# Performance work log

Measured on AMD Instinct MI355X. Metric: run time of the kernel, lower is better.

The kernel has to match this reference:

```python
import jax, jax.numpy as jnp
import numpy as np

B, QL, T, H = 32, 1, 2048, 512


def setup_inputs() -> dict:
    key = jax.random.key(0)
    ks = jax.random.split(key, 10)
    n = lambda i, shape, sc=1.0: jax.random.normal(ks[i], shape, dtype=jnp.float32) * sc
    inv = 1.0 / np.sqrt(H)
    return {
        "query": n(0, (B, QL, H)),
        "value": n(1, (B, T, H)),
        "last_attn": jax.random.uniform(ks[2], (B, T), dtype=jnp.float32),
        "conv_w": n(3, (H, 1, 3), 0.1),   # Conv1d weight (out_ch, in_ch=1, k=3)
        "conv_b": n(4, (H,), 0.1),
        "q_w": n(5, (H, H), inv),          # query_proj (no bias)
        "v_w": n(6, (H, H), inv),          # value_proj (no bias)
        "s_w": n(7, (1, H), inv),          # score_proj weight
        "s_b": n(8, (1,), 0.1),            # score_proj bias
        "bias": n(9, (H,), 0.1),           # learned additive bias
    }


def reference(query, value, last_attn, conv_w, conv_b, q_w, v_w, s_w, s_b, bias):
    Tlen = last_attn.shape[1]
    # Conv1d(in=1, out=H, k=3, pad=1) over last_attn, then transpose -> (B, T, H)
    pad = jnp.pad(last_attn, ((0, 0), (1, 1)))
    frames = jnp.stack([pad[:, k:k + Tlen] for k in range(3)], axis=0)  # (3, B, T)
    conv_attn = jnp.einsum('hk,kbt->bth', conv_w[:, 0, :], frames) + conv_b  # (B, T, H)
    q = jnp.einsum('bqh,oh->bqo', query, q_w)   # (B, 1, H)
    v = jnp.einsum('bth,oh->bto', value, v_w)   # (B, T, H)
    e = jnp.tanh(q + v + conv_attn + bias)      # (B, T, H), q broadcasts over T
    score = jnp.einsum('bth,oh->bt', e, s_w) + s_b  # (B, T)
    # smoothing=True branch: sigmoid then L1-normalize
    score = jax.nn.sigmoid(score)
    attn = score / jnp.sum(score, axis=-1, keepdims=True)
    context = jnp.einsum('bt,bth->bh', attn, value)  # bmm(attn[:,None,:], value).squeeze(1)
    return context, attn
```

## Files before the change

### kernel.cpp

```cpp
#include <hip/hip_runtime.h>
#include <math.h>

#define B 32
#define T 2048
#define H 512

#define BT2 64
#define ASTR 520

typedef __attribute__((ext_vector_type(8))) __bf16 bf16x8;
typedef __attribute__((ext_vector_type(4))) __bf16 bf16x4v;
typedef __attribute__((ext_vector_type(4))) float f32x4;
typedef __attribute__((ext_vector_type(4))) float floatx4;

union pack8 { bf16x4v h; uint2 u; };

__global__ __launch_bounds__(256) void k_init(const float* __restrict__ query,
                                              const float* __restrict__ q_w,
                                              const float* __restrict__ bias,
                                              const float* __restrict__ v_w,
                                              float* __restrict__ qpb,
                                              unsigned short* __restrict__ wbf,
                                              float* __restrict__ ctx_num,
                                              float* __restrict__ denom) {
    const int blk = blockIdx.x;
    const int tid = threadIdx.x;

    if (blk >= 544) {
#pragma unroll
        for (int i = 0; i < 16; ++i) {
            const int off = tid * 4 + i * 1024;
            *(f32x4*)(ctx_num + off) = (f32x4){0.f, 0.f, 0.f, 0.f};
        }
        if (tid < B) denom[tid] = 0.f;
        return;
    }
    if (blk >= 512) {
        const int c2 = blk - 512;
        const int wv = tid >> 6;
        const int lane = tid & 63;
        const int srow = (c2 >> 2) * 64 + (c2 & 3) * 16 + (lane & 15);
        const int scol0 = (lane >> 4) * 8;
#pragma unroll
        for (int kk = 0; kk < 4; ++kk) {
            const int k = wv * 4 + kk;
            const float* src = v_w + (size_t)srow * H + k * 32 + scol0;
            f32x4 a0 = __builtin_nontemporal_load((const f32x4*)src);
            f32x4 a1 = __builtin_nontemporal_load((const f32x4*)(src + 4));
            pack8 p0, p1;
            p0.h = __builtin_convertvector(a0, bf16x4v);
            p1.h = __builtin_convertvector(a1, bf16x4v);
            uint4 u = {p0.u.x, p0.u.y, p1.u.x, p1.u.y};
            *(uint4*)(wbf + ((size_t)c2 * 16 + k) * 512 + lane * 8) = u;
        }
        return;
    }

    const int b = blk >> 4;
    const int s = blk & 15;
    const int wave = tid >> 6;
    const int lane = tid & 63;

    const float* qb = query + (size_t)b * H + lane * 8;
    f32x4 q0 = *(const f32x4*)qb;
    f32x4 q1 = *(const f32x4*)(qb + 4);

    const int o0 = s * 32 + wave * 8;
#pragma unroll
    for (int i = 0; i < 8; ++i) {
        const int o = o0 + i;
        const float* wr = q_w + (size_t)o * H + lane * 8;
        f32x4 w0 = __builtin_nontemporal_load((const f32x4*)wr);
        f32x4 w1 = __builtin_nontemporal_load((const f32x4*)(wr + 4));
        float acc = w0.x * q0.x + w0.y * q0.y + w0.z * q0.z + w0.w * q0.w +
                    w1.x * q1.x + w1.y * q1.y + w1.z * q1.z + w1.w * q1.w;
#pragma unroll
        for (int m = 1; m < 64; m <<= 1) acc += __shfl_xor(acc, m);
        if (lane == 0) qpb[b * H + o] = acc + bias[o];
    }
}

__global__ __launch_bounds__(512, 4) void k2_fused(const float* __restrict__ value,
                                                   const unsigned short* __restrict__ wbf,
                                                   const float* __restrict__ la,
                                                   const float* __restrict__ conv_w,
                                                   const float* __restrict__ conv_b,
                                                   const float* __restrict__ s_w,
                                                   const float* __restrict__ qpb,
                                                   const float* __restrict__ s_b,
                                                   float* __restrict__ pre_sg,
                                                   float* __restrict__ ctx_num,
                                                   float* __restrict__ denom) {
    __shared__ __align__(16) unsigned short As[BT2 * ASTR];
    __shared__ float las[BT2 + 2];
    __shared__ float redp[BT2][9];
    __shared__ float sgs[BT2];
    __shared__ float redc[4][H];

    const int t0 = blockIdx.x * BT2;
    const int b  = blockIdx.y;
    const int tid = threadIdx.x;
    const int wave = tid >> 6;
    const int lane = tid & 63;
    const int tx   = lane & 15;
    const int quad = lane >> 4;
    const int wn   = wave * 64;

    if (tid < BT2 + 2) {
        const int t = t0 + tid - 1;
        las[tid] = (t >= 0 && t < T) ? la[b * T + t] : 0.f;
    }

    {
        const int srow = tid >> 3;
        const int scol = (tid & 7) * 8;
        const float* sg = value + ((size_t)b * T + t0 + srow) * H + scol;
        unsigned short* sl = &As[srow * ASTR + scol];
#pragma unroll
        for (int c = 0; c < 8; ++c) {
            f32x4 a0 = __builtin_nontemporal_load((const f32x4*)(sg + c * 64));
            f32x4 a1 = __builtin_nontemporal_load((const f32x4*)(sg + c * 64 + 4));
            pack8 p0, p1;
            p0.h = __builtin_convertvector(a0, bf16x4v);
            p1.h = __builtin_convertvector(a1, bf16x4v);
            uint4 u = {p0.u.x, p0.u.y, p1.u.x, p1.u.y};
            *(uint4*)(sl + c * 64) = u;
        }
    }
    __syncthreads();

    floatx4 acc[4][4];
#pragma unroll
    for (int i = 0; i < 4; ++i)
#pragma unroll
        for (int j = 0; j < 4; ++j) acc[i][j] = (floatx4){0.f, 0.f, 0.f, 0.f};

    const unsigned short* gB = wbf + (size_t)wave * 32768 + lane * 8;
    const unsigned short* aB = &As[tx * ASTR + quad * 8];

    bf16x8 bcur[4], bnxt[4];
#pragma unroll
    for (int ni = 0; ni < 4; ++ni)
        bcur[ni] = *(const bf16x8*)(gB + ni * 8192);

#pragma unroll
    for (int k = 0; k < 16; ++k) {
        if (k < 15) {
#pragma unroll
            for (int ni = 0; ni < 4; ++ni)
                bnxt[ni] = *(const bf16x8*)(gB + ni * 8192 + (k + 1) * 512);
        }
        bf16x8 af[4];
#pragma unroll
        for (int mi = 0; mi < 4; ++mi)
            af[mi] = *(const bf16x8*)(aB + mi * 16 * ASTR + k * 32);
#pragma unroll
        for (int mi = 0; mi < 4; ++mi)
#pragma unroll
            for (int ni = 0; ni < 4; ++ni)
                acc[mi][ni] = __builtin_amdgcn_mfma_f32_16x16x32_bf16(
                    af[mi], bcur[ni], acc[mi][ni], 0, 0, 0);
        if (k < 15) {
#pragma unroll
            for (int ni = 0; ni < 4; ++ni) bcur[ni] = bnxt[ni];
        }
    }

    float qp4[4], sw4[4], cb4[4], c04[4], c14[4], c24[4];
#pragma unroll
    for (int ni = 0; ni < 4; ++ni) {
        const int ol = wn + ni * 16 + tx;
        qp4[ni] = qpb[b * H + ol];
        sw4[ni] = s_w[ol];
        cb4[ni] = conv_b[ol];
        c04[ni] = conv_w[ol * 3 + 0];
        c14[ni] = conv_w[ol * 3 + 1];
        c24[ni] = conv_w[ol * 3 + 2];
    }

    float sacc[16];
#pragma unroll
    for (int i = 0; i < 16; ++i) sacc[i] = 0.f;
#pragma unroll
    for (int ni = 0; ni < 4; ++ni) {
#pragma unroll
        for (int mi = 0; mi < 4; ++mi)
#pragma unroll
            for (int r = 0; r < 4; ++r) {
                const int tl = mi * 16 + quad * 4 + r;
                const float conv = c04[ni] * las[tl] + c14[ni] * las[tl + 1] +
                                   c24[ni] * las[tl + 2] + cb4[ni];
                const float x = acc[mi][ni][r] + qp4[ni] + conv;
                const float ex = __expf(2.f * x);
                const float th = 1.f - 2.f * __builtin_amdgcn_rcpf(ex + 1.f);
                sacc[mi * 4 + r] += sw4[ni] * th;
            }
    }
#pragma unroll
    for (int i = 0; i < 16; ++i) {
        float v = sacc[i];
        v += __shfl_xor(v, 1);
        v += __shfl_xor(v, 2);
        v += __shfl_xor(v, 4);
        v += __shfl_xor(v, 8);
        if (tx == 0) redp[(i >> 2) * 16 + quad * 4 + (i & 3)][wave] = v;
    }
    __syncthreads();

    if (tid < BT2) {
        float sc = s_b[0];
#pragma unroll
        for (int w = 0; w < 8; ++w) sc += redp[tid][w];
        const float sg = 1.f / (1.f + __expf(-sc));
        sgs[tid] = sg;
        pre_sg[b * T + t0 + tid] = sg;
        float dsum = sg;
#pragma unroll
        for (int m = 1; m < 64; m <<= 1) dsum += __shfl_xor(dsum, m);
        if (tid == 0) atomicAdd(&denom[b], dsum);
    }
    __syncthreads();

    {
        const int h4 = (tid & 127) * 4;
        const int tp = tid >> 7;
        f32x4 a = {0.f, 0.f, 0.f, 0.f};
        for (int t = tp; t < BT2; t += 4) {
            const float w = sgs[t];
            bf16x4v hv = *(const bf16x4v*)&As[t * ASTR + h4];
            f32x4 v = __builtin_convertvector(hv, f32x4);
            a.x += w * v.x; a.y += w * v.y; a.z += w * v.z; a.w += w * v.w;
        }
        *(f32x4*)&redc[tp][h4] = a;
    }
    __syncthreads();
    if (tid < 128) {
        const int h = tid * 4;
        f32x4 r0 = *(const f32x4*)&redc[0][h];
        f32x4 r1 = *(const f32x4*)&redc[1][h];
        f32x4 r2 = *(const f32x4*)&redc[2][h];
        f32x4 r3 = *(const f32x4*)&redc[3][h];
        atomicAdd(&ctx_num[b * H + h + 0], r0.x + r1.x + r2.x + r3.x);
        atomicAdd(&ctx_num[b * H + h + 1], r0.y + r1.y + r2.y + r3.y);
        atomicAdd(&ctx_num[b * H + h + 2], r0.z + r1.z + r2.z + r3.z);
        atomicAdd(&ctx_num[b * H + h + 3], r0.w + r1.w + r2.w + r3.w);
    }
}

__global__ __launch_bounds__(256) void k3_scale(const float* __restrict__ pre_sg,
                                                const float* __restrict__ ctx_num,
                                                const float* __restrict__ denom,
                                                float* __restrict__ attn_out,
                                                float* __restrict__ ctx) {
    const int bx = blockIdx.x;
    const int b  = blockIdx.y;
    const int tid = threadIdx.x;
    const float inv = 1.f / denom[b];
    const int t = bx * 256 + tid;
    attn_out[b * T + t] = pre_sg[b * T + t] * inv;
    if (tid < 64) {
        const int h = bx * 64 + tid;
        ctx[b * H + h] = ctx_num[b * H + h] * inv;
    }
}

extern "C" void kernel_launch(void* const* d_in, const int* in_sizes, int n_in,
                              void* d_out, int out_size, void* d_ws, size_t ws_size,
                              hipStream_t stream) {
    const float* query  = (const float*)d_in[0];
    const float* value  = (const float*)d_in[1];
    const float* la     = (const float*)d_in[2];
    const float* conv_w = (const float*)d_in[3];
    const float* conv_b = (const float*)d_in[4];
    const float* q_w    = (const float*)d_in[5];
    const float* v_w    = (const float*)d_in[6];
    const float* s_w    = (const float*)d_in[7];
    const float* s_b    = (const float*)d_in[8];
    const float* bias   = (const float*)d_in[9];

    float* out  = (float*)d_out;
    float* ctx  = out;
    float* attn = out + B * H;

    float* qpb     = (float*)d_ws;
    float* pre_sg  = qpb + B * H;
    float* ctx_num = pre_sg + B * T;
    float* denom   = ctx_num + B * H;
    unsigned short* wbf = (unsigned short*)(denom + 64);

    k_init<<<545, 256, 0, stream>>>(query, q_w, bias, v_w, qpb, wbf, ctx_num, denom);

    dim3 g2(T / BT2, B);
    k2_fused<<<g2, 512, 0, stream>>>(value, wbf, la, conv_w, conv_b, s_w, qpb, s_b,
                                     pre_sg, ctx_num, denom);

    dim3 g3(8, B);
    k3_scale<<<g3, 256, 0, stream>>>(pre_sg, ctx_num, denom, attn, ctx);
}
```

Before: 249.3 us.

## Pipeline value tile staging with MFMA loop over column chunks

Instead of loading the whole 64x512 value tile into LDS before the GEMM, the kernel stages one 64-column chunk at a time. It prefetches the next chunks into registers two steps ahead and runs the MFMA over each chunk while the next one is converted and written. The aim is to hide global load latency of the value tile behind matrix math. The cost is a __syncthreads per chunk, and the register prefetch of the weight fragments across k steps is dropped.

After: 250.0 us. About the same (+0.3%).

```diff
diff --git a/kernel.cpp b/kernel.cpp
--- a/kernel.cpp
+++ b/kernel.cpp
@@ -14,6 +14,10 @@
 typedef __attribute__((ext_vector_type(4))) float floatx4;
 
 union pack8 { bf16x4v h; uint2 u; };
+
+static __device__ __forceinline__ f32x4 ntld(const float* p) {
+    return __builtin_nontemporal_load((const f32x4*)p);
+}
 
 __global__ __launch_bounds__(256) void k_init(const float* __restrict__ query,
                                               const float* __restrict__ q_w,
@@ -45,8 +49,8 @@
         for (int kk = 0; kk < 4; ++kk) {
             const int k = wv * 4 + kk;
             const float* src = v_w + (size_t)srow * H + k * 32 + scol0;
-            f32x4 a0 = __builtin_nontemporal_load((const f32x4*)src);
-            f32x4 a1 = __builtin_nontemporal_load((const f32x4*)(src + 4));
+            f32x4 a0 = ntld(src);
+            f32x4 a1 = ntld(src + 4);
             pack8 p0, p1;
             p0.h = __builtin_convertvector(a0, bf16x4v);
             p1.h = __builtin_convertvector(a1, bf16x4v);
@@ -70,8 +74,8 @@
     for (int i = 0; i < 8; ++i) {
         const int o = o0 + i;
         const float* wr = q_w + (size_t)o * H + lane * 8;
-        f32x4 w0 = __builtin_nontemporal_load((const f32x4*)wr);
-        f32x4 w1 = __builtin_nontemporal_load((const f32x4*)(wr + 4));
+        f32x4 w0 = ntld(wr);
+        f32x4 w1 = ntld(wr + 4);
         float acc = w0.x * q0.x + w0.y * q0.y + w0.z * q0.z + w0.w * q0.w +
                     w1.x * q1.x + w1.y * q1.y + w1.z * q1.z + w1.w * q1.w;
 #pragma unroll
@@ -111,21 +115,22 @@
         las[tid] = (t >= 0 && t < T) ? la[b * T + t] : 0.f;
     }
 
+    const int srow = tid >> 3;
+    const int scol = (tid & 7) * 8;
+    const float* sgp = value + ((size_t)b * T + t0 + srow) * H + scol;
+    unsigned short* slp = &As[srow * ASTR + scol];
+
+    f32x4 w0, w1;
     {
-        const int srow = tid >> 3;
-        const int scol = (tid & 7) * 8;
-        const float* sg = value + ((size_t)b * T + t0 + srow) * H + scol;
-        unsigned short* sl = &As[srow * ASTR + scol];
-#pragma unroll
-        for (int c = 0; c < 8; ++c) {
-            f32x4 a0 = __builtin_nontemporal_load((const f32x4*)(sg + c * 64));
-            f32x4 a1 = __builtin_nontemporal_load((const f32x4*)(sg + c * 64 + 4));
-            pack8 p0, p1;
-            p0.h = __builtin_convertvector(a0, bf16x4v);
-            p1.h = __builtin_convertvector(a1, bf16x4v);
-            uint4 u = {p0.u.x, p0.u.y, p1.u.x, p1.u.y};
-            *(uint4*)(sl + c * 64) = u;
-        }
+        f32x4 a0 = ntld(sgp);
+        f32x4 a1 = ntld(sgp + 4);
+        w0 = ntld(sgp + 64);
+        w1 = ntld(sgp + 68);
+        pack8 p0, p1;
+        p0.h = __builtin_convertvector(a0, bf16x4v);
+        p1.h = __builtin_convertvector(a1, bf16x4v);
+        uint4 u = {p0.u.x, p0.u.y, p1.u.x, p1.u.y};
+        *(uint4*)slp = u;
     }
     __syncthreads();
 
@@ -138,31 +143,42 @@
     const unsigned short* gB = wbf + (size_t)wave * 32768 + lane * 8;
     const unsigned short* aB = &As[tx * ASTR + quad * 8];
 
-    bf16x8 bcur[4], bnxt[4];
-#pragma unroll
-    for (int ni = 0; ni < 4; ++ni)
-        bcur[ni] = *(const bf16x8*)(gB + ni * 8192);
-
-#pragma unroll
-    for (int k = 0; k < 16; ++k) {
-        if (k < 15) {
+#pragma unroll
+    for (int c = 0; c < 8; ++c) {
+        f32x4 n0, n1;
+        if (c < 6) {
+            n0 = ntld(sgp + (c + 2) * 64);
+            n1 = ntld(sgp + (c + 2) * 64 + 4);
+        }
+
+#pragma unroll
+        for (int kk = 0; kk < 2; ++kk) {
+            const int k = c * 2 + kk;
+            bf16x8 bfr[4];
 #pragma unroll
             for (int ni = 0; ni < 4; ++ni)
-                bnxt[ni] = *(const bf16x8*)(gB + ni * 8192 + (k + 1) * 512);
-        }
-        bf16x8 af[4];
-#pragma unroll
-        for (int mi = 0; mi < 4; ++mi)
-            af[mi] = *(const bf16x8*)(aB + mi * 16 * ASTR + k * 32);
-#pragma unroll
-        for (int mi = 0; mi < 4; ++mi)
-#pragma unroll
-            for (int ni = 0; ni < 4; ++ni)
-                acc[mi][ni] = __builtin_amdgcn_mfma_f32_16x16x32_bf16(
-                    af[mi], bcur[ni], acc[mi][ni], 0, 0, 0);
-        if (k < 15) {
-#pragma unroll
-            for (int ni = 0; ni < 4; ++ni) bcur[ni] = bnxt[ni];
+                bfr[ni] = *(const bf16x8*)(gB + ni * 8192 + k * 512);
+            bf16x8 af[4];
+#pragma unroll
+            for (int mi = 0; mi < 4; ++mi)
+                af[mi] = *(const bf16x8*)(aB + mi * 16 * ASTR + k * 32);
+#pragma unroll
+            for (int mi = 0; mi < 4; ++mi)
+#pragma unroll
+                for (int ni = 0; ni < 4; ++ni)
+                    acc[mi][ni] = __builtin_amdgcn_mfma_f32_16x16x32_bf16(
+                        af[mi], bfr[ni], acc[mi][ni], 0, 0, 0);
+        }
+
+        if (c < 7) {
+            pack8 p0, p1;
+            p0.h = __builtin_convertvector(w0, bf16x4v);
+            p1.h = __builtin_convertvector(w1, bf16x4v);
+            uint4 u = {p0.u.x, p0.u.y, p1.u.x, p1.u.y};
+            *(uint4*)(slp + (c + 1) * 64) = u;
+            w0 = n0;
+            w1 = n1;
+            __syncthreads();
         }
     }
 
```
